# Performance work log

Hardware: AMD Instinct MI355X
Metric: run time of the kernel (lower is better)

The kernel has to match this reference:

```python
import jax, jax.numpy as jnp
import numpy as np

DIM = 512
HEADS = 8
DH = 64
INNER = HEADS * DH  # 512
GRID = 32
FH, FW = GRID, GRID // 2 + 1


def _group_norm1(x, g, b, eps=1e-5):
    # GroupNorm(1, C) on NHWC: normalize over (H, W, C) per sample, per-channel affine
    mu = jnp.mean(x, axis=(1, 2, 3), keepdims=True)
    var = jnp.var(x, axis=(1, 2, 3), keepdims=True)
    return (x - mu) * jax.lax.rsqrt(var + eps) * g + b


def setup_inputs() -> dict:
    key = jax.random.key(0)
    ks = jax.random.split(key, 12)
    B, N, C = 8, GRID * GRID + 1, DIM
    s = 0.02
    return {
        "x": jax.random.normal(ks[0], (B, N, C), jnp.float32),
        "Wq": jax.random.normal(ks[1], (C, INNER), jnp.float32) * s,
        "Wk": jax.random.normal(ks[2], (C, INNER), jnp.float32) * s,
        "Wv": jax.random.normal(ks[3], (C, INNER), jnp.float32) * s,
        "dw_w": jax.random.normal(ks[4], (3, 3, 1, C), jnp.float32) * s,   # depthwise, HWIO
        "pw_w": jax.random.normal(ks[5], (C, INNER), jnp.float32) * s,     # 1x1 conv
        "ln_g": jnp.ones((INNER,), jnp.float32),
        "ln_b": jnp.zeros((INNER,), jnp.float32),
        "fr_wr": jnp.ones((FH, FW, C), jnp.float32),    # learnable FFT filter (real)
        "fr_wi": jnp.zeros((FH, FW, C), jnp.float32),   # learnable FFT filter (imag)
        "fr_pw": jax.random.normal(ks[6], (C, INNER), jnp.float32) * s,
        "fr_g": jnp.ones((INNER,), jnp.float32),
        "fr_b": jnp.zeros((INNER,), jnp.float32),
        "g_W1": jax.random.normal(ks[7], (3 * INNER, 3 * INNER // 4), jnp.float32) * s,
        "g_b1": jnp.zeros((3 * INNER // 4,), jnp.float32),
        "g_W2": jax.random.normal(ks[8], (3 * INNER // 4, 3), jnp.float32) * s,
        "g_b2": jnp.zeros((3,), jnp.float32),
        "Wp": jax.random.normal(ks[9], (INNER, DIM), jnp.float32) * s,
        "bp": jnp.zeros((DIM,), jnp.float32),
        "h_feat": GRID,
        "w_feat": GRID,
    }


def reference(x, Wq, Wk, Wv, dw_w, pw_w, ln_g, ln_b, fr_wr, fr_wi, fr_pw, fr_g, fr_b,
              g_W1, g_b1, g_W2, g_b2, Wp, bp, h_feat, w_feat):
    B, N, C = x.shape
    scale = DH ** -0.5
    has_cls = (N == h_feat * w_feat + 1)
    spatial = x[:, 1:] if has_cls else x

    # Branch 1: global self-attention (manual softmax attention)
    q = (x @ Wq).reshape(B, N, HEADS, DH)
    k = (x @ Wk).reshape(B, N, HEADS, DH)
    v = (x @ Wv).reshape(B, N, HEADS, DH)
    attn = jax.nn.softmax(jnp.einsum('bihd,bjhd->bhij', q, k) * scale, axis=-1)
    glob = jnp.einsum('bhij,bjhd->bihd', attn, v).reshape(B, N, INNER)

    # Branch 2: local depthwise conv -> pointwise conv -> GroupNorm(1)
    sp = spatial.reshape(B, h_feat, w_feat, C)  # NHWC
    dw = jax.lax.conv_general_dilated(sp, dw_w, (1, 1), 'SAME',
                                      dimension_numbers=('NHWC', 'HWIO', 'NHWC'),
                                      feature_group_count=C)
    loc = _group_norm1(jnp.einsum('bhwc,co->bhwo', dw, pw_w), ln_g, ln_b)
    loc = loc.reshape(B, h_feat * w_feat, INNER)
    if has_cls:
        loc = jnp.concatenate([loc.mean(axis=1, keepdims=True), loc], axis=1)

    # Branch 3: frequency enhancement (rfft2 -> learnable complex filter -> irfft2)
    xf = jnp.fft.rfft2(sp, axes=(1, 2), norm='ortho')               # (B, FH, FW, C)
    xf = xf * jax.lax.complex(fr_wr, fr_wi)[None]
    xe = jnp.fft.irfft2(xf, s=(h_feat, w_feat), axes=(1, 2), norm='ortho')
    fr = jax.nn.gelu(_group_norm1(jnp.einsum('bhwc,co->bhwo', xe, fr_pw), fr_g, fr_b),
                     approximate=False)
    fr = fr.reshape(B, h_feat * w_feat, INNER)
    if has_cls:
        fr = jnp.concatenate([fr.mean(axis=1, keepdims=True), fr], axis=1)

    # Gate MLP + softmax fusion
    cat = jnp.concatenate([glob, loc, fr], axis=-1)                  # (B, N, 3*INNER)
    gw = jax.nn.softmax(jax.nn.gelu(cat @ g_W1 + g_b1, approximate=False) @ g_W2 + g_b2,
                        axis=-1)                                     # (B, N, 3)
    fused = gw[..., 0:1] * glob + gw[..., 1:2] * loc + gw[..., 2:3] * fr
    return fused @ Wp + bp
```

## Files before the change

### kernel.cpp

```cpp
#include <hip/hip_runtime.h>
#include <math.h>

#define BB 8
#define NT 1025
#define CD 512
#define NH 8
#define DHD 64
#define HW 1024
#define FWD 17
#define MTOK 8200
#define MPAD 8320
#define QKS 1536

typedef __attribute__((ext_vector_type(8))) short short8;
typedef __attribute__((ext_vector_type(4))) float f32x4;
typedef __attribute__((ext_vector_type(16))) float f32x16;
typedef __attribute__((ext_vector_type(4))) unsigned u32x4;

__device__ __forceinline__ float gelu_exact(float x){
  return 0.5f * x * (1.0f + erff(x * 0.70710678118654752f));
}

__device__ __forceinline__ short f2bf(float f){
  unsigned u = __float_as_uint(f);
  unsigned r = (u + 0x7FFFu + ((u >> 16) & 1u)) >> 16;
  return (short)r;
}

__device__ __forceinline__ float bf2f(short s){
  unsigned u = ((unsigned)(unsigned short)s) << 16;
  return __uint_as_float(u);
}

__device__ __forceinline__ unsigned cvt_pk_bf16(float lo, float hi){
  unsigned r;
  asm volatile("v_cvt_pk_bf16_f32 %0, %1, %2" : "=v"(r) : "v"(lo), "v"(hi));
  return r;
}

typedef const __attribute__((address_space(1))) unsigned GASu;
typedef __attribute__((address_space(3))) unsigned LASu;
__device__ __forceinline__ void gload16(const void* g, void* l){
  __builtin_amdgcn_global_load_lds((GASu*)g, (LASu*)l, 16, 0, 0);
}

__device__ __forceinline__ int xcd_logical(int phys, int n){
  int xcd = phys & 7, slot = phys >> 3;
  int q = n >> 3, r = n & 7;
  return xcd*q + (xcd < r ? xcd : r) + slot;
}

__global__ __launch_bounds__(256) void wconv_all(
    const float* __restrict__ Wq, const float* __restrict__ Wk, const float* __restrict__ Wv,
    const float* __restrict__ pw, const float* __restrict__ frpw,
    const float* __restrict__ gW1, const float* __restrict__ Wp,
    short* __restrict__ wqkvt, short* __restrict__ pwt, short* __restrict__ frpwt,
    short* __restrict__ gw1t, short* __restrict__ wpt)
{
  const int t = blockIdx.x;
  const float* W; short* Wt; int K, N, idx; float scale = 1.0f;
  if      (t < 256) { W = Wq;   Wt = wqkvt;            K=512;  N=512; idx=t;       scale=0.125f; }
  else if (t < 512) { W = Wk;   Wt = wqkvt+512*512;    K=512;  N=512; idx=t-256; }
  else if (t < 768) { W = Wv;   Wt = wqkvt+1024*512;   K=512;  N=512; idx=t-512; }
  else if (t < 1024){ W = pw;   Wt = pwt;              K=512;  N=512; idx=t-768; }
  else if (t < 1280){ W = frpw; Wt = frpwt;            K=512;  N=512; idx=t-1024; }
  else if (t < 1856){ W = gW1;  Wt = gw1t;             K=1536; N=384; idx=t-1280; }
  else              { W = Wp;   Wt = wpt;              K=512;  N=512; idx=t-1856; }
  const int ntn = N >> 5;
  const int n0 = (idx % ntn) << 5, k0 = (idx / ntn) << 5;
  __shared__ float tl[32][33];
  const int tx = threadIdx.x & 31, ty = threadIdx.x >> 5;
  #pragma unroll
  for (int i = 0; i < 32; i += 8)
    tl[ty+i][tx] = W[(size_t)(k0+ty+i)*N + n0+tx];
  __syncthreads();
  #pragma unroll
  for (int i = 0; i < 32; i += 8)
    Wt[(size_t)(n0+ty+i)*K + k0+tx] = f2bf(tl[tx][ty+i] * scale);
}

__global__ __launch_bounds__(256) void x2bf(const float* __restrict__ x, short* __restrict__ xb)
{
  size_t i = ((size_t)blockIdx.x*256 + threadIdx.x) * 8;
  if (i >= (size_t)MPAD*CD) return;
  size_t row = i >> 9;
  short8 o;
  if (row < MTOK){
    #pragma unroll
    for (int j = 0; j < 8; j++) o[j] = f2bf(x[i+j]);
  } else {
    #pragma unroll
    for (int j = 0; j < 8; j++) o[j] = 0;
  }
  *(short8*)(xb + i) = o;
}


#define GEMM_DECL                                                          \
  __shared__ short As[2][128*64];                                          \
  __shared__ short Bs[2][64*64];                                           \
  const int tid = threadIdx.x;                                             \
  const int lane = tid & 63, wv = tid >> 6;                                \
  const int lc = lane & 15, lg = lane >> 4;                                \
  f32x4 acc[2][4];                                                         \
  _Pragma("unroll")                                                        \
  for (int rt=0;rt<2;rt++)                                                 \
    _Pragma("unroll")                                                      \
    for (int ct=0;ct<4;ct++) acc[rt][ct] = (f32x4){0.f,0.f,0.f,0.f};

#define GEMM_ISSUE(Aptr, Ka, k0a, Bptr, Kb, k0b, buf)                      \
  _Pragma("unroll")                                                        \
  for (int p = 0; p < 4; p++){                                             \
    int r0 = wv*32 + p*8;                                                  \
    int r = r0 + (lane>>3), s = lane & 7;                                  \
    gload16((Aptr) + (size_t)(row0 + r)*(Ka) + (k0a) + ((s ^ (r&7))*8),    \
            &As[buf][r0*64]);                                              \
  }                                                                        \
  _Pragma("unroll")                                                        \
  for (int p = 0; p < 2; p++){                                             \
    int r0 = wv*16 + p*8;                                                  \
    int r = r0 + (lane>>3), s = lane & 7;                                  \
    gload16((Bptr) + (size_t)(col0 + r)*(Kb) + (k0b) + ((s ^ (r&7))*8),    \
            &Bs[buf][r0*64]);                                              \
  }

#define GEMM_COMPUTE(buf)                                                  \
  _Pragma("unroll")                                                        \
  for (int ks = 0; ks < 2; ks++){                                          \
    short8 af[2], bfr[4];                                                  \
    _Pragma("unroll")                                                      \
    for (int rt = 0; rt < 2; rt++){                                        \
      int r = wv*32 + rt*16 + lc;                                          \
      af[rt] = *(const short8*)&As[buf][r*64 + (((ks*4+lg) ^ (r & 7))*8)]; \
    }                                                                      \
    _Pragma("unroll")                                                      \
    for (int ct = 0; ct < 4; ct++){                                        \
      int r = ct*16 + lc;                                                  \
      bfr[ct] = *(const short8*)&Bs[buf][r*64 + (((ks*4+lg) ^ (r & 7))*8)];\
    }                                                                      \
    _Pragma("unroll")                                                      \
    for (int rt = 0; rt < 2; rt++)                                         \
      _Pragma("unroll")                                                    \
      for (int ct = 0; ct < 4; ct++)                                       \
        acc[rt][ct] = __builtin_amdgcn_mfma_f32_16x16x32_bf16(af[rt], bfr[ct], acc[rt][ct], 0,0,0); \
  }

__global__ __launch_bounds__(256) void gemm_bf16(
    const short* __restrict__ A, const short* __restrict__ Bt,
    const float* __restrict__ bias, void* __restrict__ Cm,
    int M, int N, int K, int flags)
{
  const int l = xcd_logical(blockIdx.x, gridDim.x);
  const int nx = N >> 6;
  const int row0 = (l / nx) * 128, col0 = (l % nx) * 64;
  GEMM_DECL;

  const int nk = K >> 6;
  GEMM_ISSUE(A, K, 0, Bt, K, 0, 0);
  __syncthreads();
  for (int kt = 0; kt < nk; kt++){
    const int cur = kt & 1;
    if (kt + 1 < nk){ GEMM_ISSUE(A, K, (kt+1)*64, Bt, K, (kt+1)*64, cur ^ 1); }
    GEMM_COMPUTE(cur);
    if (kt + 1 < nk) __syncthreads();
  }

  #pragma unroll
  for (int rt = 0; rt < 2; rt++)
    #pragma unroll
    for (int e = 0; e < 4; e++){
      int gr = row0 + wv*32 + rt*16 + lg*4 + e;
      if (gr >= M) continue;
      #pragma unroll
      for (int ct = 0; ct < 4; ct++){
        int gc = col0 + ct*16 + lc;
        float v = acc[rt][ct][e];
        if (flags & 1) v += bias[gc];
        if (flags & 2) v = gelu_exact(v);
        if (flags & 4) ((short*)Cm)[(size_t)gr*N + gc] = f2bf(v);
        else           ((float*)Cm)[(size_t)gr*N + gc] = v;
      }
    }
}

__global__ __launch_bounds__(256) void gemm_pw2(
    const short* __restrict__ A0, const short* __restrict__ B0,
    const short* __restrict__ A1, const short* __restrict__ B1,
    short* __restrict__ C0, short* __restrict__ C1,
    float* __restrict__ totL, float* __restrict__ totF)
{
  const int l = xcd_logical(blockIdx.x, 1024);
  const int bx = l & 7;
  const int by = (l >> 3) & 63;
  const int br = l >> 9;
  const short* A  = br ? A1 : A0;
  const short* Bt = br ? B1 : B0;
  short* Cm       = br ? C1 : C0;
  float* tot      = br ? totF : totL;
  const int N = 512, K = 512;
  const int row0 = by * 128, col0 = bx * 64;
  GEMM_DECL;

  const int nk = 8;
  GEMM_ISSUE(A, K, 0, Bt, K, 0, 0);
  __syncthreads();
  for (int kt = 0; kt < nk; kt++){
    const int cur = kt & 1;
    if (kt + 1 < nk){ GEMM_ISSUE(A, K, (kt+1)*64, Bt, K, (kt+1)*64, cur ^ 1); }
    GEMM_COMPUTE(cur);
    if (kt + 1 < nk) __syncthreads();
  }

  float s1 = 0.f, s2 = 0.f;
  #pragma unroll
  for (int rt = 0; rt < 2; rt++)
    #pragma unroll
    for (int e = 0; e < 4; e++){
      int gr = row0 + wv*32 + rt*16 + lg*4 + e;
      #pragma unroll
      for (int ct = 0; ct < 4; ct++){
        int gc = col0 + ct*16 + lc;
        float v = acc[rt][ct][e];
        Cm[(size_t)gr*N + gc] = f2bf(v);
        s1 += v; s2 += v*v;
      }
    }
  #pragma unroll
  for (int o = 32; o > 0; o >>= 1){ s1 += __shfl_xor(s1, o); s2 += __shfl_xor(s2, o); }
  if (lane == 0){
    atomicAdd(&tot[(row0>>10)*2],   s1);
    atomicAdd(&tot[(row0>>10)*2+1], s2);
  }
}

__global__ __launch_bounds__(256) void gemm_gate(
    const short* __restrict__ A0, const short* __restrict__ A1, const short* __restrict__ A2,
    const short* __restrict__ Bt, const float* __restrict__ bias, short* __restrict__ Cm,
    int M)
{
  const int N = 384, K = 1536;
  const int l = xcd_logical(blockIdx.x, gridDim.x);
  const int row0 = (l / 6) * 128, col0 = (l % 6) * 64;
  GEMM_DECL;

  const int nk = 24;
  {
    const short* Asrc = A0;
    GEMM_ISSUE(Asrc, 512, 0, Bt, K, 0, 0);
  }
  __syncthreads();
  for (int kt = 0; kt < nk; kt++){
    const int cur = kt & 1;
    if (kt + 1 < nk){
      int k0 = (kt+1) * 64;
      const short* Asrc = (k0 < 512) ? A0 : (k0 < 1024 ? A1 : A2);
      const int kb = k0 & 511;
      GEMM_ISSUE(Asrc, 512, kb, Bt, K, k0, cur ^ 1);
    }
    GEMM_COMPUTE(cur);
    if (kt + 1 < nk) __syncthreads();
  }

  #pragma unroll
  for (int rt = 0; rt < 2; rt++)
    #pragma unroll
    for (int e = 0; e < 4; e++){
      int gr = row0 + wv*32 + rt*16 + lg*4 + e;
      if (gr >= M) continue;
      #pragma unroll
      for (int ct = 0; ct < 4; ct++){
        int gc = col0 + ct*16 + lc;
        float v = acc[rt][ct][e] + bias[gc];
        Cm[(size_t)gr*N + gc] = f2bf(gelu_exact(v));
      }
    }
}

__global__ __launch_bounds__(256) void attn_mfma32(
    const short* __restrict__ qkv, short* __restrict__ glob)
{
  const int bi = blockIdx.x;
  const int xcd = bi & 7;
  const int jj = bi >> 3;
  const int gq = jj / 9;
  const int qt = jj - gq*9;
  const int g  = xcd + 8*gq;
  const int h  = g & 7, b = g >> 3;

  const int tid = threadIdx.x;
  const int lane = tid & 63, wq = tid >> 6;
  const int q32 = lane & 31;
  const int hi  = lane >> 5;
  const int bN = b * NT;
  const int q0w = qt*128 + wq*32;

  __shared__ short Kl[2][64*64];
  __shared__ short Vl[2][64*64];

  short8 qf[4];
  {
    int qr = q0w + q32; if (qr > 1024) qr = 1024;
    const short* qp = qkv + (size_t)(bN + qr)*QKS + h*DHD + hi*8;
    qf[0] = *(const short8*)(qp);
    qf[1] = *(const short8*)(qp + 16);
    qf[2] = *(const short8*)(qp + 32);
    qf[3] = *(const short8*)(qp + 48);
  }

  f32x16 oA = {0.f,0.f,0.f,0.f,0.f,0.f,0.f,0.f,0.f,0.f,0.f,0.f,0.f,0.f,0.f,0.f};
  f32x16 oB = oA;
  float rs = 0.f;

  const int kc0 = tid;
  const int kc1 = tid + 256;
  const int vkey = tid & 63, vdg = tid >> 6;
  const short* kgbase = qkv + (size_t)bN*QKS + 512 + h*DHD;
  const short* vgbase = qkv + (size_t)bN*QKS + 1024 + h*DHD;

  short8 gk0, gk1, gv0, gv1;
  auto loadT = [&](int kt2){
    gk0 = *(const short8*)(kgbase + (size_t)(kt2*64 + (kc0>>3))*QKS + (kc0&7)*8);
    gk1 = *(const short8*)(kgbase + (size_t)(kt2*64 + (kc1>>3))*QKS + (kc1&7)*8);
    gv0 = *(const short8*)(vgbase + (size_t)(kt2*64 + vkey)*QKS + vdg*16);
    gv1 = *(const short8*)(vgbase + (size_t)(kt2*64 + vkey)*QKS + vdg*16 + 8);
  };
  auto writeT = [&](int buf){
    { int r = kc0>>3, sl = kc0&7;
      *(short8*)&Kl[buf][r*64 + (((sl) ^ (r&7))*8)] = gk0; }
    { int r = kc1>>3, sl = kc1&7;
      *(short8*)&Kl[buf][r*64 + (((sl) ^ (r&7))*8)] = gk1; }
    #pragma unroll
    for (int i2 = 0; i2 < 8; i2++){
      int d0 = vdg*16 + i2, d1 = vdg*16 + 8 + i2;
      Vl[buf][d0*64 + (((vkey>>3) ^ (d0&7))*8) + (vkey&7)] = gv0[i2];
      Vl[buf][d1*64 + (((vkey>>3) ^ (d1&7))*8) + (vkey&7)] = gv1[i2];
    }
  };

  loadT(0);
  writeT(0);
  __syncthreads();

  for (int kt = 0; kt < 17; kt++){
    const int cur = kt & 1;
    if (kt < 16) loadT(kt+1);

    #pragma unroll
    for (int ks = 0; ks < 2; ks++){
      f32x16 s = {0.f,0.f,0.f,0.f,0.f,0.f,0.f,0.f,0.f,0.f,0.f,0.f,0.f,0.f,0.f,0.f};
      const int krow = ks*32 + q32;
      const int kbase = krow*64;
      const int kx = q32 & 7;
      __builtin_amdgcn_s_setprio(1);
      #pragma unroll
      for (int kk = 0; kk < 4; kk++){
        short8 af = *(const short8*)&Kl[cur][kbase + (((2*kk+hi) ^ kx)*8)];
        s = __builtin_amdgcn_mfma_f32_32x32x16_bf16(af, qf[kk], s, 0,0,0);
      }
      __builtin_amdgcn_s_setprio(0);
      float p[16];
      if (kt == 16){
        #pragma unroll
        for (int e = 0; e < 16; e++){
          bool valid = (ks == 0) && (e == 0) && (hi == 0);
          p[e] = valid ? __expf(s[e]) : 0.f;
        }
      } else {
        #pragma unroll
        for (int e = 0; e < 16; e++) p[e] = __expf(s[e]);
      }
      #pragma unroll
      for (int e = 0; e < 16; e++) rs += p[e];
      unsigned pk[4][2];
      #pragma unroll
      for (int g2 = 0; g2 < 4; g2++){
        pk[g2][0] = cvt_pk_bf16(p[4*g2+0], p[4*g2+1]);
        pk[g2][1] = cvt_pk_bf16(p[4*g2+2], p[4*g2+3]);
      }
      #pragma unroll
      for (int kc = 0; kc < 2; kc++){
        unsigned e00 = pk[2*kc][0],   e01 = pk[2*kc][1];
        unsigned e10 = pk[2*kc+1][0], e11 = pk[2*kc+1][1];
        unsigned t00 = (unsigned)__shfl_xor((int)e00, 32);
        unsigned t01 = (unsigned)__shfl_xor((int)e01, 32);
        unsigned t10 = (unsigned)__shfl_xor((int)e10, 32);
        unsigned t11 = (unsigned)__shfl_xor((int)e11, 32);
        u32x4 pu;
        pu[0] = hi ? t10 : e00;
        pu[1] = hi ? t11 : e01;
        pu[2] = hi ? e10 : t00;
        pu[3] = hi ? e11 : t01;
        short8 pa = *(short8*)&pu;
        const int vsl = 4*ks + 2*kc + hi;
        __builtin_amdgcn_s_setprio(1);
        {
          short8 vf0 = *(const short8*)&Vl[cur][(q32)*64      + ((vsl ^ kx)*8)];
          oA = __builtin_amdgcn_mfma_f32_32x32x16_bf16(pa, vf0, oA, 0,0,0);
          short8 vf1 = *(const short8*)&Vl[cur][(32+q32)*64   + ((vsl ^ kx)*8)];
          oB = __builtin_amdgcn_mfma_f32_32x32x16_bf16(pa, vf1, oB, 0,0,0);
        }
        __builtin_amdgcn_s_setprio(0);
      }
    }

    if (kt < 16){
      writeT(cur ^ 1);
      __syncthreads();
    }
  }

  float rs_tot = rs + __shfl_xor(rs, 32);
  #pragma unroll
  for (int e = 0; e < 16; e++){
    int rowr = (e & 3) + 8*(e >> 2) + 4*hi;
    int q = q0w + rowr;
    if (q > 1024) continue;
    float inv = 1.0f / __shfl(rs_tot, rowr);
    size_t base = (size_t)(bN + q)*CD + h*DHD + q32;
    glob[base]      = f2bf(oA[e] * inv);
    glob[base + 32] = f2bf(oB[e] * inv);
  }
}

__global__ __launch_bounds__(512) void dwconv(
    const short* __restrict__ xb, const float* __restrict__ w, short* __restrict__ out)
{
  const int c = threadIdx.x;
  const int xx = blockIdx.x & 31;
  const int yg = (blockIdx.x >> 5) & 7;
  const int b  = blockIdx.x >> 8;
  const int y0 = yg << 2;
  float acc[4] = {0.f,0.f,0.f,0.f};
  #pragma unroll
  for (int dx = -1; dx <= 1; dx++){
    int x2 = xx + dx;
    if (x2 < 0 || x2 > 31) continue;
    float col[6];
    #pragma unroll
    for (int r = 0; r < 6; r++){
      int row = y0 - 1 + r;
      col[r] = (row >= 0 && row < 32)
             ? bf2f(xb[((size_t)(b*NT + 1 + row*32 + x2))*CD + c]) : 0.f;
    }
    float w0 = w[(0*3+dx+1)*CD + c];
    float w1 = w[(1*3+dx+1)*CD + c];
    float w2 = w[(2*3+dx+1)*CD + c];
    #pragma unroll
    for (int o = 0; o < 4; o++)
      acc[o] += col[o]*w0 + col[o+1]*w1 + col[o+2]*w2;
  }
  #pragma unroll
  for (int o = 0; o < 4; o++)
    out[((size_t)(b*HW + (y0+o)*32 + xx))*CD + c] = f2bf(acc[o]);
}

__global__ __launch_bounds__(512) void gn_apply2(
    const short* __restrict__ mmL, const short* __restrict__ mmF,
    const float* __restrict__ totL, const float* __restrict__ totF,
    const float* __restrict__ gL, const float* __restrict__ bL,
    const float* __restrict__ gF, const float* __restrict__ bF,
    short* __restrict__ loc, short* __restrict__ fr,
    float* __restrict__ colsumL, float* __restrict__ colsumF)
{
  const int br = blockIdx.x >> 8;
  const int bi = blockIdx.x & 255;
  const int c = threadIdx.x;
  const int b = bi >> 5;
  const int p0 = (bi & 31) << 5;
  const short* mm = br ? mmF : mmL;
  const float* tot = br ? totF : totL;
  short* out = br ? fr : loc;
  float* colsum = br ? colsumF : colsumL;
  const float inv = 1.0f / ((float)HW * CD);
  const float mu = tot[b*2] * inv;
  const float rstd = rsqrtf(tot[b*2+1]*inv - mu*mu + 1e-5f);
  const float gc = (br ? gF : gL)[c], bc = (br ? bF : bL)[c];
  float s = 0.0f;
  for (int r = 0; r < 32; r++){
    int p = p0 + r;
    float v = bf2f(mm[((size_t)b*HW + p)*CD + c]);
    v = (v - mu) * rstd * gc + bc;
    if (br) v = gelu_exact(v);
    out[((size_t)(b*NT + 1 + p))*CD + c] = f2bf(v);
    s += v;
  }
  atomicAdd(&colsum[b*CD + c], s);
}

__global__ __launch_bounds__(512) void colmean_fin2(
    const float* __restrict__ colsumL, const float* __restrict__ colsumF,
    short* __restrict__ loc, short* __restrict__ fr)
{
  const int c = threadIdx.x;
  const int b = blockIdx.x & 7;
  if (blockIdx.x < 8) loc[((size_t)b*NT)*CD + c] = f2bf(colsumL[b*CD + c] * (1.0f/HW));
  else                fr [((size_t)b*NT)*CD + c] = f2bf(colsumF[b*CD + c] * (1.0f/HW));
}

__global__ __launch_bounds__(512) void fft_f1(
    const float* __restrict__ x, float* __restrict__ Ur, float* __restrict__ Ui)
{
  const int c = threadIdx.x;
  const int xx = blockIdx.x & 31;
  const int b = blockIdx.x >> 5;
  __shared__ float ct[32], st[32];
  if (c < 32){ float ang = 6.283185307179586f * c / 32.0f; ct[c] = cosf(ang); st[c] = sinf(ang); }
  __syncthreads();
  float v[32];
  #pragma unroll
  for (int y = 0; y < 32; y++) v[y] = x[((size_t)(b*NT + 1 + y*32 + xx))*CD + c];
  for (int ky = 0; ky <= 16; ky++){
    float sr = 0.f, si = 0.f;
    #pragma unroll
    for (int y = 0; y < 32; y++){
      int idx = (ky*y) & 31;
      sr += v[y]*ct[idx]; si -= v[y]*st[idx];
    }
    size_t o = ((size_t)((b*17+ky)*32+xx))*CD + c;
    Ur[o] = sr; Ui[o] = si;
  }
}

__global__ __launch_bounds__(256) void fft_f2(
    const float* __restrict__ Ur, const float* __restrict__ Ui,
    const float* __restrict__ wr, const float* __restrict__ wi,
    float* __restrict__ Gr, float* __restrict__ Gi)
{
  const int c = (blockIdx.x & 1)*256 + threadIdx.x;
  const int t = blockIdx.x >> 1;
  const int ky = t % 17, b = t / 17;
  __shared__ float ct[32], st[32];
  if (threadIdx.x < 32){ float ang = 6.283185307179586f * threadIdx.x / 32.0f;
    ct[threadIdx.x] = cosf(ang); st[threadIdx.x] = sinf(ang); }
  __syncthreads();
  float ar[32], ai[32];
  #pragma unroll
  for (int kx = 0; kx < 32; kx++){ ar[kx] = 0.f; ai[kx] = 0.f; }
  #pragma unroll
  for (int xx = 0; xx < 32; xx++){
    size_t o = ((size_t)((b*17+ky)*32+xx))*CD + c;
    float ur = Ur[o], ui = Ui[o];
    #pragma unroll
    for (int kx = 0; kx < 32; kx++){
      int idx = (kx*xx) & 31;
      float cc = ct[idx], ss = st[idx];
      ar[kx] += ur*cc + ui*ss;
      ai[kx] += ui*cc - ur*ss;
    }
  }
  #pragma unroll
  for (int kx = 0; kx < FWD; kx++){
    size_t fo = ((size_t)(ky*FWD+kx))*CD + c;
    float fwr = wr[fo], fwi = wi[fo];
    size_t go = ((size_t)((b*17+kx)*32+ky))*CD + c;
    Gr[go] = ar[kx]*fwr - ai[kx]*fwi;
    Gi[go] = ar[kx]*fwi + ai[kx]*fwr;
  }
  if (ky >= 1 && ky <= 15){
    const int ky2 = 32 - ky;
    #pragma unroll
    for (int kx = 0; kx < FWD; kx++){
      int m = (32 - kx) & 31;
      size_t fo = ((size_t)(ky2*FWD+kx))*CD + c;
      float fwr = wr[fo], fwi = wi[fo];
      size_t go = ((size_t)((b*17+kx)*32+ky2))*CD + c;
      Gr[go] = ar[m]*fwr + ai[m]*fwi;
      Gi[go] = ar[m]*fwi - ai[m]*fwr;
    }
  }
}

__global__ __launch_bounds__(256) void fft_f3(
    const float* __restrict__ Gr, const float* __restrict__ Gi,
    float* __restrict__ Tr, float* __restrict__ Ti)
{
  const int c = (blockIdx.x & 1)*256 + threadIdx.x;
  const int t = blockIdx.x >> 1;
  const int kx = t % 17, b = t / 17;
  __shared__ float ct[32], st[32];
  if (threadIdx.x < 32){ float ang = 6.283185307179586f * threadIdx.x / 32.0f;
    ct[threadIdx.x] = cosf(ang); st[threadIdx.x] = sinf(ang); }
  __syncthreads();
  float tr[32], ti[32];
  #pragma unroll
  for (int y = 0; y < 32; y++){ tr[y] = 0.f; ti[y] = 0.f; }
  #pragma unroll
  for (int ky = 0; ky < 32; ky++){
    size_t go = ((size_t)((b*17+kx)*32+ky))*CD + c;
    float gr = Gr[go], gi = Gi[go];
    #pragma unroll
    for (int y = 0; y < 32; y++){
      int idx = (ky*y) & 31;
      float cc = ct[idx], ss = st[idx];
      tr[y] += gr*cc - gi*ss;
      ti[y] += gr*ss + gi*cc;
    }
  }
  #pragma unroll
  for (int y = 0; y < 32; y++){
    size_t to = ((size_t)((b*32+y)*17+kx))*CD + c;
    Tr[to] = tr[y]*(1.0f/32.0f);
    Ti[to] = ti[y]*(1.0f/32.0f);
  }
}

__global__ __launch_bounds__(512) void fft_f4(
    const float* __restrict__ Tr, const float* __restrict__ Ti, short* __restrict__ xe)
{
  const int c = threadIdx.x;
  const int y = blockIdx.x & 31;
  const int b = blockIdx.x >> 5;
  __shared__ float ct[32], st[32];
  if (c < 32){ float ang = 6.283185307179586f * c / 32.0f; ct[c] = cosf(ang); st[c] = sinf(ang); }
  __syncthreads();
  float tr[FWD], ti[FWD];
  #pragma unroll
  for (int kx = 0; kx < FWD; kx++){
    size_t o = ((size_t)((b*32+y)*17+kx))*CD + c;
    tr[kx] = Tr[o]; ti[kx] = Ti[o];
  }
  for (int x2 = 0; x2 < 32; x2++){
    float acc = tr[0] + ((x2 & 1) ? -tr[16] : tr[16]);
    #pragma unroll
    for (int k2 = 1; k2 < 16; k2++){
      int idx = (k2*x2) & 31;
      acc += 2.0f*(tr[k2]*ct[idx] - ti[k2]*st[idx]);
    }
    xe[((size_t)(b*HW + y*32 + x2))*CD + c] = f2bf(acc*(1.0f/32.0f));
  }
}

__global__ __launch_bounds__(256) void gate_fuse(
    const short* __restrict__ h1, const float* __restrict__ gW2, const float* __restrict__ gb2,
    const short* __restrict__ glob, const short* __restrict__ loc, const short* __restrict__ fr,
    short* __restrict__ fused)
{
  const int token = blockIdx.x*4 + (threadIdx.x >> 6);
  const int lane = threadIdx.x & 63;
  if (token >= MTOK) return;
  float p0 = 0.f, p1 = 0.f, p2 = 0.f;
  #pragma unroll
  for (int i = 0; i < 6; i++){
    int idx = lane + i*64;
    float h = bf2f(h1[(size_t)token*384 + idx]);
    p0 += h * gW2[idx*3+0]; p1 += h * gW2[idx*3+1]; p2 += h * gW2[idx*3+2];
  }
  #pragma unroll
  for (int o = 32; o > 0; o >>= 1){
    p0 += __shfl_xor(p0, o); p1 += __shfl_xor(p1, o); p2 += __shfl_xor(p2, o);
  }
  p0 += gb2[0]; p1 += gb2[1]; p2 += gb2[2];
  float mx = fmaxf(p0, fmaxf(p1, p2));
  float e0 = __expf(p0-mx), e1 = __expf(p1-mx), e2 = __expf(p2-mx);
  float inv = 1.0f/(e0+e1+e2);
  float g0 = e0*inv, g1 = e1*inv, g2 = e2*inv;
  #pragma unroll
  for (int i = 0; i < 8; i++){
    size_t o2 = (size_t)token*CD + lane + i*64;
    fused[o2] = f2bf(g0*bf2f(glob[o2]) + g1*bf2f(loc[o2]) + g2*bf2f(fr[o2]));
  }
}

extern "C" void kernel_launch(void* const* d_in, const int* in_sizes, int n_in,
                              void* d_out, int out_size, void* d_ws, size_t ws_size,
                              hipStream_t stream)
{
  const float* x     = (const float*)d_in[0];
  const float* Wq    = (const float*)d_in[1];
  const float* Wk    = (const float*)d_in[2];
  const float* Wv    = (const float*)d_in[3];
  const float* dw_w  = (const float*)d_in[4];
  const float* pw_w  = (const float*)d_in[5];
  const float* ln_g  = (const float*)d_in[6];
  const float* ln_b  = (const float*)d_in[7];
  const float* fr_wr = (const float*)d_in[8];
  const float* fr_wi = (const float*)d_in[9];
  const float* fr_pw = (const float*)d_in[10];
  const float* fr_g  = (const float*)d_in[11];
  const float* fr_b  = (const float*)d_in[12];
  const float* g_W1  = (const float*)d_in[13];
  const float* g_b1  = (const float*)d_in[14];
  const float* g_W2  = (const float*)d_in[15];
  const float* g_b2  = (const float*)d_in[16];
  const float* Wp    = (const float*)d_in[17];
  const float* bp    = (const float*)d_in[18];

  float* ws = (float*)d_ws;
  float* scrA = ws;
  float* scrB = scrA + 8388608;
  float* stats = scrB + 4456448;
  float* totL    = stats;
  float* totF    = stats + 16;
  float* colsumL = stats + 64;
  float* colsumF = stats + 64 + 4096;

  const size_t RPAD = 8448;
  short* glob  = (short*)(stats + 16384);
  short* loc   = glob  + RPAD*CD;
  short* fr    = loc   + RPAD*CD;
  short* actbL = fr    + RPAD*CD;
  short* actbF = actbL + RPAD*CD;
  short* fused = actbL;
  short* qkvb  = actbF + RPAD*CD;
  short* xb    = qkvb + (size_t)MPAD*QKS;
  short* wqkvt = xb + (size_t)MPAD*CD;
  short* pwt   = wqkvt + 1536*512;
  short* frpwt = pwt + 512*512;
  short* gw1t  = frpwt + 512*512;
  short* wpt   = gw1t + 384*1536;
  short* mmL = (short*)scrA;
  short* mmF = mmL + (size_t)8192*CD;

  hipMemsetAsync(stats, 0, (64 + 2*4096)*sizeof(float), stream);
  wconv_all<<<2112, 256, 0, stream>>>(Wq, Wk, Wv, pw_w, fr_pw, g_W1, Wp,
                                      wqkvt, pwt, frpwt, gw1t, wpt);
  x2bf<<<2080, 256, 0, stream>>>(x, xb);

  gemm_bf16<<<1560, 256, 0, stream>>>(xb, wqkvt, nullptr, qkvb, MPAD, 1536, 512, 4);
  attn_mfma32<<<576, 256, 0, stream>>>(qkvb, glob);

  dwconv<<<BB*8*32, 512, 0, stream>>>(xb, dw_w, actbL);
  float* Ur = scrA;            float* Ui = scrA + 2228224;
  float* Gr = scrB;            float* Gi = scrB + 2228224;
  float* Tr = scrA;            float* Ti = scrA + 2228224;
  fft_f1<<<BB*32, 512, 0, stream>>>(x, Ur, Ui);
  fft_f2<<<BB*17*2, 256, 0, stream>>>(Ur, Ui, fr_wr, fr_wi, Gr, Gi);
  fft_f3<<<BB*17*2, 256, 0, stream>>>(Gr, Gi, Tr, Ti);
  fft_f4<<<BB*32, 512, 0, stream>>>(Tr, Ti, actbF);

  gemm_pw2<<<1024, 256, 0, stream>>>(actbL, pwt, actbF, frpwt, mmL, mmF, totL, totF);

  gn_apply2<<<512, 512, 0, stream>>>(mmL, mmF, totL, totF, ln_g, ln_b, fr_g, fr_b,
                                     loc, fr, colsumL, colsumF);
  colmean_fin2<<<16, 512, 0, stream>>>(colsumL, colsumF, loc, fr);

  gemm_gate<<<390, 256, 0, stream>>>(glob, loc, fr, gw1t, g_b1, (short*)scrB, MTOK);
  gate_fuse<<<2050, 256, 0, stream>>>((short*)scrB, g_W2, g_b2, glob, loc, fr, fused);
  gemm_bf16<<<520, 256, 0, stream>>>(fused, wpt, bp, d_out, MTOK, 512, 512, 1);
}
```

Before: 324.7 us.

## Merge prep kernels and QKV/pointwise GEMMs into single launches; drop async LDS loads

Folds the weight transpose, x-to-bf16 conversion and stats memset into one prep launch. Merges the QKV projection GEMM with the two pointwise-conv GEMMs into one larger grid, and moves the attention launch after it. Every GEMM's double-buffered global_load_lds staging is replaced by a single-buffer register load/store with a barrier on both sides of each stage. This cuts launch count and tail effects but loses the copy/compute overlap, so the GEMM main loops may stall more on memory.

```diff
diff --git a/kernel.cpp b/kernel.cpp
--- a/kernel.cpp
+++ b/kernel.cpp
@@ -38,26 +38,45 @@
   return r;
 }
 
-typedef const __attribute__((address_space(1))) unsigned GASu;
-typedef __attribute__((address_space(3))) unsigned LASu;
-__device__ __forceinline__ void gload16(const void* g, void* l){
-  __builtin_amdgcn_global_load_lds((GASu*)g, (LASu*)l, 16, 0, 0);
-}
-
 __device__ __forceinline__ int xcd_logical(int phys, int n){
   int xcd = phys & 7, slot = phys >> 3;
   int q = n >> 3, r = n & 7;
   return xcd*q + (xcd < r ? xcd : r) + slot;
 }
 
-__global__ __launch_bounds__(256) void wconv_all(
+__global__ __launch_bounds__(256) void prep_all(
     const float* __restrict__ Wq, const float* __restrict__ Wk, const float* __restrict__ Wv,
     const float* __restrict__ pw, const float* __restrict__ frpw,
     const float* __restrict__ gW1, const float* __restrict__ Wp,
     short* __restrict__ wqkvt, short* __restrict__ pwt, short* __restrict__ frpwt,
-    short* __restrict__ gw1t, short* __restrict__ wpt)
+    short* __restrict__ gw1t, short* __restrict__ wpt,
+    const float* __restrict__ x, short* __restrict__ xb, float* __restrict__ stats)
 {
   const int t = blockIdx.x;
+  if (t >= 4192){
+    int i0 = (t - 4192)*1024 + threadIdx.x;
+    #pragma unroll
+    for (int j = 0; j < 4; j++){
+      int i = i0 + j*256;
+      if (i < 8256) stats[i] = 0.f;
+    }
+    return;
+  }
+  if (t >= 2112){
+    size_t i = ((size_t)(t - 2112)*256 + threadIdx.x) * 8;
+    if (i >= (size_t)MPAD*CD) return;
+    size_t row = i >> 9;
+    short8 o;
+    if (row < MTOK){
+      #pragma unroll
+      for (int j = 0; j < 8; j++) o[j] = f2bf(x[i+j]);
+    } else {
+      #pragma unroll
+      for (int j = 0; j < 8; j++) o[j] = 0;
+    }
+    *(short8*)(xb + i) = o;
+    return;
+  }
   const float* W; short* Wt; int K, N, idx; float scale = 1.0f;
   if      (t < 256) { W = Wq;   Wt = wqkvt;            K=512;  N=512; idx=t;       scale=0.125f; }
   else if (t < 512) { W = Wk;   Wt = wqkvt+512*512;    K=512;  N=512; idx=t-256; }
@@ -79,26 +98,9 @@
     Wt[(size_t)(n0+ty+i)*K + k0+tx] = f2bf(tl[tx][ty+i] * scale);
 }
 
-__global__ __launch_bounds__(256) void x2bf(const float* __restrict__ x, short* __restrict__ xb)
-{
-  size_t i = ((size_t)blockIdx.x*256 + threadIdx.x) * 8;
-  if (i >= (size_t)MPAD*CD) return;
-  size_t row = i >> 9;
-  short8 o;
-  if (row < MTOK){
-    #pragma unroll
-    for (int j = 0; j < 8; j++) o[j] = f2bf(x[i+j]);
-  } else {
-    #pragma unroll
-    for (int j = 0; j < 8; j++) o[j] = 0;
-  }
-  *(short8*)(xb + i) = o;
-}
-
-
 #define GEMM_DECL                                                          \
-  __shared__ short As[2][128*64];                                          \
-  __shared__ short Bs[2][64*64];                                           \
+  __shared__ short As[128*64];                                             \
+  __shared__ short Bs[64*64];                                              \
   const int tid = threadIdx.x;                                             \
   const int lane = tid & 63, wv = tid >> 6;                                \
   const int lc = lane & 15, lg = lane >> 4;                                \
@@ -108,35 +110,37 @@
     _Pragma("unroll")                                                      \
     for (int ct=0;ct<4;ct++) acc[rt][ct] = (f32x4){0.f,0.f,0.f,0.f};
 
-#define GEMM_ISSUE(Aptr, Ka, k0a, Bptr, Kb, k0b, buf)                      \
+#define GEMM_STAGE(Aptr, Ka, k0a, Bptr, Kb, k0b)                           \
+  __syncthreads();                                                         \
   _Pragma("unroll")                                                        \
   for (int p = 0; p < 4; p++){                                             \
-    int r0 = wv*32 + p*8;                                                  \
-    int r = r0 + (lane>>3), s = lane & 7;                                  \
-    gload16((Aptr) + (size_t)(row0 + r)*(Ka) + (k0a) + ((s ^ (r&7))*8),    \
-            &As[buf][r0*64]);                                              \
+    int c = tid + p*256;                                                   \
+    int r = c >> 3, s = c & 7;                                             \
+    short8 v = *(const short8*)((Aptr) + (size_t)(row0 + r)*(Ka) + (k0a) + s*8); \
+    *(short8*)&As[r*64 + ((s ^ (r & 7))*8)] = v;                           \
   }                                                                        \
   _Pragma("unroll")                                                        \
   for (int p = 0; p < 2; p++){                                             \
-    int r0 = wv*16 + p*8;                                                  \
-    int r = r0 + (lane>>3), s = lane & 7;                                  \
-    gload16((Bptr) + (size_t)(col0 + r)*(Kb) + (k0b) + ((s ^ (r&7))*8),    \
-            &Bs[buf][r0*64]);                                              \
-  }
-
-#define GEMM_COMPUTE(buf)                                                  \
+    int c = tid + p*256;                                                   \
+    int r = c >> 3, s = c & 7;                                             \
+    short8 v = *(const short8*)((Bptr) + (size_t)(col0 + r)*(Kb) + (k0b) + s*8); \
+    *(short8*)&Bs[r*64 + ((s ^ (r & 7))*8)] = v;                           \
+  }                                                                        \
+  __syncthreads();
+
+#define GEMM_COMPUTE                                                       \
   _Pragma("unroll")                                                        \
   for (int ks = 0; ks < 2; ks++){                                          \
     short8 af[2], bfr[4];                                                  \
     _Pragma("unroll")                                                      \
     for (int rt = 0; rt < 2; rt++){                                        \
       int r = wv*32 + rt*16 + lc;                                          \
-      af[rt] = *(const short8*)&As[buf][r*64 + (((ks*4+lg) ^ (r & 7))*8)]; \
+      af[rt] = *(const short8*)&As[r*64 + (((ks*4+lg) ^ (r & 7))*8)];      \
     }                                                                      \
     _Pragma("unroll")                                                      \
     for (int ct = 0; ct < 4; ct++){                                        \
       int r = ct*16 + lc;                                                  \
-      bfr[ct] = *(const short8*)&Bs[buf][r*64 + (((ks*4+lg) ^ (r & 7))*8)];\
+      bfr[ct] = *(const short8*)&Bs[r*64 + (((ks*4+lg) ^ (r & 7))*8)];     \
     }                                                                      \
     _Pragma("unroll")                                                      \
     for (int rt = 0; rt < 2; rt++)                                         \
@@ -145,72 +149,34 @@
         acc[rt][ct] = __builtin_amdgcn_mfma_f32_16x16x32_bf16(af[rt], bfr[ct], acc[rt][ct], 0,0,0); \
   }
 
-__global__ __launch_bounds__(256) void gemm_bf16(
-    const short* __restrict__ A, const short* __restrict__ Bt,
-    const float* __restrict__ bias, void* __restrict__ Cm,
-    int M, int N, int K, int flags)
-{
-  const int l = xcd_logical(blockIdx.x, gridDim.x);
-  const int nx = N >> 6;
-  const int row0 = (l / nx) * 128, col0 = (l % nx) * 64;
+__global__ __launch_bounds__(256) void gemm_mega(
+    const short* __restrict__ xb, const short* __restrict__ wqkvt, short* __restrict__ qkvb,
+    const short* __restrict__ aL, const short* __restrict__ bL, short* __restrict__ cL,
+    float* __restrict__ totL,
+    const short* __restrict__ aF, const short* __restrict__ bF, short* __restrict__ cF,
+    float* __restrict__ totF)
+{
+  const int l = xcd_logical(blockIdx.x, 2584);
+  const short *A, *Bt; short* Cm; float* tot = nullptr;
+  int N, row0, col0;
+  if (l < 1560){
+    A = xb; Bt = wqkvt; Cm = qkvb; N = 1536;
+    row0 = (l / 24) * 128; col0 = (l % 24) * 64;
+  } else if (l < 2072){
+    int l2 = l - 1560;
+    A = aL; Bt = bL; Cm = cL; tot = totL; N = 512;
+    row0 = (l2 >> 3) * 128; col0 = (l2 & 7) * 64;
+  } else {
+    int l2 = l - 2072;
+    A = aF; Bt = bF; Cm = cF; tot = totF; N = 512;
+    row0 = (l2 >> 3) * 128; col0 = (l2 & 7) * 64;
+  }
+  const int K = 512;
   GEMM_DECL;
-
-  const int nk = K >> 6;
-  GEMM_ISSUE(A, K, 0, Bt, K, 0, 0);
-  __syncthreads();
-  for (int kt = 0; kt < nk; kt++){
-    const int cur = kt & 1;
-    if (kt + 1 < nk){ GEMM_ISSUE(A, K, (kt+1)*64, Bt, K, (kt+1)*64, cur ^ 1); }
-    GEMM_COMPUTE(cur);
-    if (kt + 1 < nk) __syncthreads();
-  }
-
-  #pragma unroll
-  for (int rt = 0; rt < 2; rt++)
-    #pragma unroll
-    for (int e = 0; e < 4; e++){
-      int gr = row0 + wv*32 + rt*16 + lg*4 + e;
-      if (gr >= M) continue;
-      #pragma unroll
-      for (int ct = 0; ct < 4; ct++){
-        int gc = col0 + ct*16 + lc;
-        float v = acc[rt][ct][e];
-        if (flags & 1) v += bias[gc];
-        if (flags & 2) v = gelu_exact(v);
-        if (flags & 4) ((short*)Cm)[(size_t)gr*N + gc] = f2bf(v);
-        else           ((float*)Cm)[(size_t)gr*N + gc] = v;
-      }
-    }
-}
-
-__global__ __launch_bounds__(256) void gemm_pw2(
-    const short* __restrict__ A0, const short* __restrict__ B0,
-    const short* __restrict__ A1, const short* __restrict__ B1,
-    short* __restrict__ C0, short* __restrict__ C1,
-    float* __restrict__ totL, float* __restrict__ totF)
-{
-  const int l = xcd_logical(blockIdx.x, 1024);
-  const int bx = l & 7;
-  const int by = (l >> 3) & 63;
-  const int br = l >> 9;
-  const short* A  = br ? A1 : A0;
-  const short* Bt = br ? B1 : B0;
-  short* Cm       = br ? C1 : C0;
-  float* tot      = br ? totF : totL;
-  const int N = 512, K = 512;
-  const int row0 = by * 128, col0 = bx * 64;
-  GEMM_DECL;
-
-  const int nk = 8;
-  GEMM_ISSUE(A, K, 0, Bt, K, 0, 0);
-  __syncthreads();
-  for (int kt = 0; kt < nk; kt++){
-    const int cur = kt & 1;
-    if (kt + 1 < nk){ GEMM_ISSUE(A, K, (kt+1)*64, Bt, K, (kt+1)*64, cur ^ 1); }
-    GEMM_COMPUTE(cur);
-    if (kt + 1 < nk) __syncthreads();
-  }
-
+  for (int k0 = 0; k0 < K; k0 += 64){
+    GEMM_STAGE(A, K, k0, Bt, K, k0);
+    GEMM_COMPUTE;
+  }
   float s1 = 0.f, s2 = 0.f;
   #pragma unroll
   for (int rt = 0; rt < 2; rt++)
@@ -225,12 +191,40 @@
         s1 += v; s2 += v*v;
       }
     }
-  #pragma unroll
-  for (int o = 32; o > 0; o >>= 1){ s1 += __shfl_xor(s1, o); s2 += __shfl_xor(s2, o); }
-  if (lane == 0){
-    atomicAdd(&tot[(row0>>10)*2],   s1);
-    atomicAdd(&tot[(row0>>10)*2+1], s2);
-  }
+  if (tot){
+    #pragma unroll
+    for (int o = 32; o > 0; o >>= 1){ s1 += __shfl_xor(s1, o); s2 += __shfl_xor(s2, o); }
+    if (lane == 0){
+      atomicAdd(&tot[(row0>>10)*2],   s1);
+      atomicAdd(&tot[(row0>>10)*2+1], s2);
+    }
+  }
+}
+
+__global__ __launch_bounds__(256) void gemm_final(
+    const short* __restrict__ A, const short* __restrict__ Bt,
+    const float* __restrict__ bias, float* __restrict__ Cm, int M)
+{
+  const int N = 512, K = 512;
+  const int l = xcd_logical(blockIdx.x, gridDim.x);
+  const int row0 = (l >> 3) * 128, col0 = (l & 7) * 64;
+  GEMM_DECL;
+  for (int k0 = 0; k0 < K; k0 += 64){
+    GEMM_STAGE(A, K, k0, Bt, K, k0);
+    GEMM_COMPUTE;
+  }
+  #pragma unroll
+  for (int rt = 0; rt < 2; rt++)
+    #pragma unroll
+    for (int e = 0; e < 4; e++){
+      int gr = row0 + wv*32 + rt*16 + lg*4 + e;
+      if (gr >= M) continue;
+      #pragma unroll
+      for (int ct = 0; ct < 4; ct++){
+        int gc = col0 + ct*16 + lc;
+        Cm[(size_t)gr*N + gc] = acc[rt][ct][e] + bias[gc];
+      }
+    }
 }
 
 __global__ __launch_bounds__(256) void gemm_gate(
@@ -242,25 +236,13 @@
   const int l = xcd_logical(blockIdx.x, gridDim.x);
   const int row0 = (l / 6) * 128, col0 = (l % 6) * 64;
   GEMM_DECL;
-
-  const int nk = 24;
-  {
-    const short* Asrc = A0;
-    GEMM_ISSUE(Asrc, 512, 0, Bt, K, 0, 0);
-  }
-  __syncthreads();
-  for (int kt = 0; kt < nk; kt++){
-    const int cur = kt & 1;
-    if (kt + 1 < nk){
-      int k0 = (kt+1) * 64;
-      const short* Asrc = (k0 < 512) ? A0 : (k0 < 1024 ? A1 : A2);
-      const int kb = k0 & 511;
-      GEMM_ISSUE(Asrc, 512, kb, Bt, K, k0, cur ^ 1);
-    }
-    GEMM_COMPUTE(cur);
-    if (kt + 1 < nk) __syncthreads();
-  }
-
+  for (int kt = 0; kt < 24; kt++){
+    int k0 = kt * 64;
+    const short* Asrc = (k0 < 512) ? A0 : (k0 < 1024 ? A1 : A2);
+    const int kb = k0 & 511;
+    GEMM_STAGE(Asrc, 512, kb, Bt, K, k0);
+    GEMM_COMPUTE;
+  }
   #pragma unroll
   for (int rt = 0; rt < 2; rt++)
     #pragma unroll
@@ -711,13 +693,8 @@
   short* mmL = (short*)scrA;
   short* mmF = mmL + (size_t)8192*CD;
 
-  hipMemsetAsync(stats, 0, (64 + 2*4096)*sizeof(float), stream);
-  wconv_all<<<2112, 256, 0, stream>>>(Wq, Wk, Wv, pw_w, fr_pw, g_W1, Wp,
-                                      wqkvt, pwt, frpwt, gw1t, wpt);
-  x2bf<<<2080, 256, 0, stream>>>(x, xb);
-
-  gemm_bf16<<<1560, 256, 0, stream>>>(xb, wqkvt, nullptr, qkvb, MPAD, 1536, 512, 4);
-  attn_mfma32<<<576, 256, 0, stream>>>(qkvb, glob);
+  prep_all<<<4201, 256, 0, stream>>>(Wq, Wk, Wv, pw_w, fr_pw, g_W1, Wp,
+                                     wqkvt, pwt, frpwt, gw1t, wpt, x, xb, stats);
 
   dwconv<<<BB*8*32, 512, 0, stream>>>(xb, dw_w, actbL);
   float* Ur = scrA;            float* Ui = scrA + 2228224;
@@ -728,7 +705,11 @@
   fft_f3<<<BB*17*2, 256, 0, stream>>>(Gr, Gi, Tr, Ti);
   fft_f4<<<BB*32, 512, 0, stream>>>(Tr, Ti, actbF);
 
-  gemm_pw2<<<1024, 256, 0, stream>>>(actbL, pwt, actbF, frpwt, mmL, mmF, totL, totF);
+  gemm_mega<<<2584, 256, 0, stream>>>(xb, wqkvt, qkvb,
+                                      actbL, pwt, mmL, totL,
+                                      actbF, frpwt, mmF, totF);
+
+  attn_mfma32<<<576, 256, 0, stream>>>(qkvb, glob);
 
   gn_apply2<<<512, 512, 0, stream>>>(mmL, mmF, totL, totF, ln_g, ln_b, fr_g, fr_b,
                                      loc, fr, colsumL, colsumF);
@@ -736,5 +717,5 @@
 
   gemm_gate<<<390, 256, 0, stream>>>(glob, loc, fr, gw1t, g_b1, (short*)scrB, MTOK);
   gate_fuse<<<2050, 256, 0, stream>>>((short*)scrB, g_W2, g_b2, glob, loc, fr, fused);
-  gemm_bf16<<<520, 256, 0, stream>>>(fused, wpt, bp, d_out, MTOK, 512, 512, 1);
-}
+  gemm_final<<<520, 256, 0, stream>>>(fused, wpt, bp, (float*)d_out, MTOK);
+}
```

Result: faster. 307.3 us (-5.4%).
